# Kernel optimization log

Hardware: AMD Instinct MI355X
Metric: run time of the kernel (lower is better)

Reference implementation:

```python
import jax, jax.numpy as jnp
import numpy as np

H = 8      # hidden_size
IN = 14    # input_size
B = 4096   # batch
T = 512    # seq_len
BN_EPS = 1e-5


def setup_inputs() -> dict:
    key = jax.random.key(0)
    ks = jax.random.split(key, 16)
    s = lambda k, shape, scale=0.25: jax.random.normal(k, shape, jnp.float32) * scale
    return {
        "x": jax.random.normal(ks[0], (B, T, IN), jnp.float32),
        # layer 1 LSTM params (PyTorch gate order: i, f, g, o)
        "Wih1": s(ks[1], (4 * H, IN)), "Whh1": s(ks[2], (4 * H, H)),
        "bih1": s(ks[3], (4 * H,)), "bhh1": s(ks[4], (4 * H,)),
        # layer 2 LSTM params
        "Wih2": s(ks[5], (4 * H, H)), "Whh2": s(ks[6], (4 * H, H)),
        "bih2": s(ks[7], (4 * H,)), "bhh2": s(ks[8], (4 * H,)),
        # BatchNorm1d(H) params + running stats (eval mode)
        "bn_gamma": jnp.ones((H,), jnp.float32), "bn_beta": jnp.zeros((H,), jnp.float32),
        "bn_mean": s(ks[9], (H,), 0.01), "bn_var": jnp.ones((H,), jnp.float32),
        # MLP head
        "w1": s(ks[10], (4, H)), "b1": s(ks[11], (4,)),
        "w2": s(ks[12], (1, 4)), "b2": s(ks[13], (1,)),
    }


def _cell(gates, c):
    # gates: [B, 4H] pre-activation, PyTorch order i, f, g, o
    i, f, g, o = jnp.split(gates, 4, axis=-1)
    c_new = jax.nn.sigmoid(f) * c + jax.nn.sigmoid(i) * jnp.tanh(g)
    h_new = jax.nn.sigmoid(o) * jnp.tanh(c_new)
    return h_new, c_new


def _lstm_last(x, Wih1, Whh1, bih1, bhh1, Wih2, Whh2, bih2, bhh2):
    # x: [B, T, IN] -> returns last hidden state of layer 2: [B, H]
    xt = jnp.swapaxes(x, 0, 1)  # [T, B, IN]
    # precompute input projections for layer 1 in one big GEMM
    xp1 = jnp.einsum('tbf,gf->tbg', xt, Wih1) + (bih1 + bhh1)  # [T, B, 4H]
    b2sum = bih2 + bhh2
    Bn = x.shape[0]
    z = jnp.zeros((Bn, H), x.dtype)
    init = (z, z, z, z)  # h1, c1, h2, c2

    def step(carry, xp):
        h1, c1, h2, c2 = carry
        h1, c1 = _cell(xp + h1 @ Whh1.T, c1)
        h2, c2 = _cell(h1 @ Wih2.T + h2 @ Whh2.T + b2sum, c2)
        return (h1, c1, h2, c2), None

    (h1, c1, h2, c2), _ = jax.lax.scan(step, init, xp1)
    return h2


def reference(x, Wih1, Whh1, bih1, bhh1, Wih2, Whh2, bih2, bhh2,
              bn_gamma, bn_beta, bn_mean, bn_var, w1, b1, w2, b2):
    last = _lstm_last(x, Wih1, Whh1, bih1, bhh1, Wih2, Whh2, bih2, bhh2)  # [B, H]
    # BatchNorm1d in eval mode (running stats); dropout is identity in eval
    normed = bn_gamma * (last - bn_mean) / jnp.sqrt(bn_var + BN_EPS) + bn_beta
    h = jax.nn.relu(normed @ w1.T + b1)  # [B, 4]
    out = h @ w2.T + b2                  # [B, 1]
    return out.squeeze(-1)               # [B]
```

## Files before the change

### kernel.cpp

```cpp
#include <hip/hip_runtime.h>

#define T_SEQ 512
#define INPUT 14
#define HID 8
#define TC 16
#define NCHUNK (T_SEQ / TC)
#define BN_EPS 1e-5f

__device__ __forceinline__ float fast_exp2(float x) { return __builtin_amdgcn_exp2f(x); }
__device__ __forceinline__ float fast_rcp(float x)  { return __builtin_amdgcn_rcpf(x); }

template <int IMM>
__device__ __forceinline__ float swz(float v) {
    return __int_as_float(__builtin_amdgcn_ds_swizzle(__float_as_int(v), IMM));
}

#define DPP_XOR1 0xB1
#define DPP_XOR2 0x4E
#define DPP_XOR3 0x1B
#define DPP_XOR8 0x128
template <int CTRL>
__device__ __forceinline__ float dpp(float v) {
    return __int_as_float(__builtin_amdgcn_update_dpp(
        0, __float_as_int(v), CTRL, 0xF, 0xF, true));
}

__device__ __forceinline__ void butterfly8u(float h, float (&hx)[8]) {
    hx[0] = h;
    float x4  = swz<0x101F>(h);
    float x16 = swz<0x401F>(h);
    float x20 = swz<0x501F>(h);
    hx[1] = x4;
    hx[2] = dpp<DPP_XOR8>(h);
    hx[3] = dpp<DPP_XOR8>(x4);
    hx[4] = x16;
    hx[5] = x20;
    hx[6] = dpp<DPP_XOR8>(x16);
    hx[7] = dpp<DPP_XOR8>(x20);
}

__global__ __launch_bounds__(256, 2)
void lstm_forex_kernel(const float* __restrict__ x,
                       const float* __restrict__ Wih1, const float* __restrict__ Whh1,
                       const float* __restrict__ bih1, const float* __restrict__ bhh1,
                       const float* __restrict__ Wih2, const float* __restrict__ Whh2,
                       const float* __restrict__ bih2, const float* __restrict__ bhh2,
                       const float* __restrict__ bn_gamma, const float* __restrict__ bn_beta,
                       const float* __restrict__ bn_mean, const float* __restrict__ bn_var,
                       const float* __restrict__ w1p, const float* __restrict__ b1p,
                       const float* __restrict__ w2p, const float* __restrict__ b2p,
                       float* __restrict__ out)
{
    __shared__ float xbuf[4][2][TC][16];

    const int tid  = threadIdx.x;
    const int wave = tid >> 6;
    const int lane = tid & 63;
    const int grp  = lane >> 5;
    const int l5   = lane & 31;
    const int u    = (l5 >> 2) & 7;
    const int type = l5 & 3;
    const int row  = type * 8 + u;
    const bool b0  = (type & 1) != 0;
    const bool b1  = (type & 2) != 0;

    const int b = blockIdx.x * 8 + wave * 2 + grp;

    float wi1[INPUT], wh1p[8], wi2p[8], wh2p[8];
#pragma unroll
    for (int k = 0; k < INPUT; ++k) wi1[k] = Wih1[row * INPUT + k];
#pragma unroll
    for (int m = 0; m < 8; ++m) {
        int j = u ^ m;
        wh1p[m] = Whh1[row * HID + j];
        wi2p[m] = Wih2[row * HID + j];
        wh2p[m] = Whh2[row * HID + j];
    }
    const float bsum1 = bih1[row] + bhh1[row];
    const float bsum2 = bih2[row] + bhh2[row];

    const float actScale = (type == 2) ? -2.885390082f : -1.4426950408f;
    const float actMul   = (type == 2) ? 2.f : 1.f;
    const float actAdd   = (type == 2) ? -1.f : 0.f;

    const float* gptr[7];
    int loff[7];
#pragma unroll
    for (int it = 0; it < 7; ++it) {
        int d   = it * 64 + lane;
        int es  = d / 224;
        int idx = d - es * 224;
        int tr  = idx / 14;
        int k   = idx - tr * 14;
        int bb  = blockIdx.x * 8 + wave * 2 + es;
        gptr[it] = x + (size_t)bb * (T_SEQ * INPUT) + idx;
        loff[it] = es * (TC * 16) + tr * 16 + k;
    }

    float hx1[8], hx2[8];
    float c1 = 0.f, c2 = 0.f;
#pragma unroll
    for (int m = 0; m < 8; ++m) { hx1[m] = 0.f; hx2[m] = 0.f; }

    float st[7];
#pragma unroll
    for (int it = 0; it < 7; ++it) { st[it] = *gptr[it]; gptr[it] += TC * INPUT; }

    float (*xw)[TC][16] = xbuf[wave];

    for (int c = 0; c < NCHUNK; ++c) {
#pragma unroll
        for (int it = 0; it < 7; ++it) ((float*)xw)[loff[it]] = st[it];
        if (c + 1 < NCHUNK) {
#pragma unroll
            for (int it = 0; it < 7; ++it) { st[it] = *gptr[it]; gptr[it] += TC * INPUT; }
        }
        __builtin_amdgcn_wave_barrier();

#pragma unroll
        for (int t = 0; t < TC; ++t) {
            const float* xrow = &xw[grp][t][0];
            float4 xa = *(const float4*)(xrow + 0);
            float4 xb = *(const float4*)(xrow + 4);
            float4 xc = *(const float4*)(xrow + 8);
            float2 xd = *(const float2*)(xrow + 12);

            float a0 = bsum1, a1 = 0.f;
            a0 = fmaf(xa.x, wi1[0], a0);  a1 = fmaf(xa.y, wi1[1], a1);
            a0 = fmaf(xa.z, wi1[2], a0);  a1 = fmaf(xa.w, wi1[3], a1);
            a0 = fmaf(xb.x, wi1[4], a0);  a1 = fmaf(xb.y, wi1[5], a1);
            a0 = fmaf(xb.z, wi1[6], a0);  a1 = fmaf(xb.w, wi1[7], a1);
            a0 = fmaf(xc.x, wi1[8], a0);  a1 = fmaf(xc.y, wi1[9], a1);
            a0 = fmaf(xc.z, wi1[10], a0); a1 = fmaf(xc.w, wi1[11], a1);
            a0 = fmaf(xd.x, wi1[12], a0); a1 = fmaf(xd.y, wi1[13], a1);
            float q0 = bsum2, q1 = 0.f;
#pragma unroll
            for (int m = 0; m < 8; m += 2) {
                q0 = fmaf(hx2[m],     wh2p[m],     q0);
                q1 = fmaf(hx2[m + 1], wh2p[m + 1], q1);
            }
#pragma unroll
            for (int m = 0; m < 8; m += 2) {
                a0 = fmaf(hx1[m],     wh1p[m],     a0);
                a1 = fmaf(hx1[m + 1], wh1p[m + 1], a1);
            }
            float acc = a0 + a1;

            float v0 = fmaf(fast_rcp(1.f + fast_exp2(actScale * acc)), actMul, actAdd);
            float v1 = dpp<DPP_XOR1>(v0);
            float v2 = dpp<DPP_XOR2>(v0);
            float v3 = dpp<DPP_XOR3>(v0);
            float P = b0 ? v1 * v3 : v0 * v2;
            float A = b0 ? v0 : v1;
            float Bq = b0 ? v2 : v3;
            float F = b1 ? Bq : A;
            float O = b1 ? A : Bq;
            c1 = fmaf(F, c1, P);
            float th1 = fmaf(fast_rcp(1.f + fast_exp2(-2.885390082f * c1)), 2.f, -1.f);
            float h1u = O * th1;
            butterfly8u(h1u, hx1);

            float p0 = q0, p1 = q1;
#pragma unroll
            for (int m = 0; m < 8; m += 2) {
                p0 = fmaf(hx1[m],     wi2p[m],     p0);
                p1 = fmaf(hx1[m + 1], wi2p[m + 1], p1);
            }
            float acc2 = p0 + p1;

            float u0 = fmaf(fast_rcp(1.f + fast_exp2(actScale * acc2)), actMul, actAdd);
            float u1 = dpp<DPP_XOR1>(u0);
            float u2 = dpp<DPP_XOR2>(u0);
            float u3 = dpp<DPP_XOR3>(u0);
            float P2 = b0 ? u1 * u3 : u0 * u2;
            float A2 = b0 ? u0 : u1;
            float B2 = b0 ? u2 : u3;
            float F2 = b1 ? B2 : A2;
            float O2 = b1 ? A2 : B2;
            c2 = fmaf(F2, c2, P2);
            float th2 = fmaf(fast_rcp(1.f + fast_exp2(-2.885390082f * c2)), 2.f, -1.f);
            float h2u = O2 * th2;
            butterfly8u(h2u, hx2);
        }
    }

    if (l5 == 0) {
        float nd[HID];
#pragma unroll
        for (int j = 0; j < HID; ++j) {
            float inv = 1.f / sqrtf(bn_var[j] + BN_EPS);
            nd[j] = bn_gamma[j] * (hx2[j] - bn_mean[j]) * inv + bn_beta[j];
        }
        float acc = b2p[0];
#pragma unroll
        for (int m = 0; m < 4; ++m) {
            float s = b1p[m];
#pragma unroll
            for (int j = 0; j < HID; ++j) s = fmaf(nd[j], w1p[m * HID + j], s);
            s = fmaxf(s, 0.f);
            acc = fmaf(s, w2p[m], acc);
        }
        out[b] = acc;
    }
}

extern "C" void kernel_launch(void* const* d_in, const int* in_sizes, int n_in,
                              void* d_out, int out_size, void* d_ws, size_t ws_size,
                              hipStream_t stream) {
    const float* x        = (const float*)d_in[0];
    const float* Wih1     = (const float*)d_in[1];
    const float* Whh1     = (const float*)d_in[2];
    const float* bih1     = (const float*)d_in[3];
    const float* bhh1     = (const float*)d_in[4];
    const float* Wih2     = (const float*)d_in[5];
    const float* Whh2     = (const float*)d_in[6];
    const float* bih2     = (const float*)d_in[7];
    const float* bhh2     = (const float*)d_in[8];
    const float* bn_gamma = (const float*)d_in[9];
    const float* bn_beta  = (const float*)d_in[10];
    const float* bn_mean  = (const float*)d_in[11];
    const float* bn_var   = (const float*)d_in[12];
    const float* w1p      = (const float*)d_in[13];
    const float* b1p      = (const float*)d_in[14];
    const float* w2p      = (const float*)d_in[15];
    const float* b2p      = (const float*)d_in[16];
    float* out = (float*)d_out;

    const int B = in_sizes[0] / (T_SEQ * INPUT);
    dim3 grid(B / 8), block(256);
    hipLaunchKernelGGL(lstm_forex_kernel, grid, block, 0, stream,
                       x, Wih1, Whh1, bih1, bhh1, Wih2, Whh2, bih2, bhh2,
                       bn_gamma, bn_beta, bn_mean, bn_var, w1p, b1p, w2p, b2p, out);
}
```

Baseline: 339.8 us.

## Fold activation scales into weights, broadcast gates via DPP, pack input FMAs

Measured after the change: 328.7 us. 3.3% less time.

```diff
diff --git a/kernel.cpp b/kernel.cpp
--- a/kernel.cpp
+++ b/kernel.cpp
@@ -7,17 +7,31 @@
 #define NCHUNK (T_SEQ / TC)
 #define BN_EPS 1e-5f
 
+typedef float v2f __attribute__((ext_vector_type(2)));
+
 __device__ __forceinline__ float fast_exp2(float x) { return __builtin_amdgcn_exp2f(x); }
 __device__ __forceinline__ float fast_rcp(float x)  { return __builtin_amdgcn_rcpf(x); }
+
+__device__ __forceinline__ v2f pk_fma(v2f a, v2f b, v2f c) {
+    v2f d;
+    asm("v_pk_fma_f32 %0, %1, %2, %3" : "=v"(d) : "v"(a), "v"(b), "v"(c));
+    return d;
+}
+__device__ __forceinline__ v2f pk_mul(v2f a, v2f b) {
+    v2f d;
+    asm("v_pk_mul_f32 %0, %1, %2" : "=v"(d) : "v"(a), "v"(b));
+    return d;
+}
 
 template <int IMM>
 __device__ __forceinline__ float swz(float v) {
     return __int_as_float(__builtin_amdgcn_ds_swizzle(__float_as_int(v), IMM));
 }
 
-#define DPP_XOR1 0xB1
-#define DPP_XOR2 0x4E
-#define DPP_XOR3 0x1B
+#define DPP_BC0  0x00
+#define DPP_BC1  0x55
+#define DPP_BC2  0xAA
+#define DPP_BC3  0xFF
 #define DPP_XOR8 0x128
 template <int CTRL>
 __device__ __forceinline__ float dpp(float v) {
@@ -61,27 +75,30 @@
     const int u    = (l5 >> 2) & 7;
     const int type = l5 & 3;
     const int row  = type * 8 + u;
-    const bool b0  = (type & 1) != 0;
-    const bool b1  = (type & 2) != 0;
 
     const int b = blockIdx.x * 8 + wave * 2 + grp;
 
-    float wi1[INPUT], wh1p[8], wi2p[8], wh2p[8];
-#pragma unroll
-    for (int k = 0; k < INPUT; ++k) wi1[k] = Wih1[row * INPUT + k];
+    const float gateScale = (type == 2) ? -2.885390082f : -1.4426950408f;
+    const float actMul    = (type == 2) ? -5.770780164f : 1.f;
+    const float actAdd    = (type == 2) ?  2.885390082f : 0.f;
+
+    v2f   wi1p[7];
+    float wh1p[8], wi2p[8], wh2p[8];
+#pragma unroll
+    for (int k = 0; k < 7; ++k) {
+        wi1p[k] = (v2f){ Wih1[row * INPUT + 2 * k]     * gateScale,
+                         Wih1[row * INPUT + 2 * k + 1] * gateScale };
+    }
 #pragma unroll
     for (int m = 0; m < 8; ++m) {
         int j = u ^ m;
-        wh1p[m] = Whh1[row * HID + j];
-        wi2p[m] = Wih2[row * HID + j];
-        wh2p[m] = Whh2[row * HID + j];
-    }
-    const float bsum1 = bih1[row] + bhh1[row];
-    const float bsum2 = bih2[row] + bhh2[row];
-
-    const float actScale = (type == 2) ? -2.885390082f : -1.4426950408f;
-    const float actMul   = (type == 2) ? 2.f : 1.f;
-    const float actAdd   = (type == 2) ? -1.f : 0.f;
+        wh1p[m] = Whh1[row * HID + j] * gateScale;
+        wi2p[m] = Wih2[row * HID + j] * gateScale;
+        wh2p[m] = Whh2[row * HID + j] * gateScale;
+    }
+    const float bsum1s = (bih1[row] + bhh1[row]) * gateScale;
+    const float bsum2s = (bih2[row] + bhh2[row]) * gateScale;
+    const v2f   bias1  = { bsum1s, 0.f };
 
     const float* gptr[7];
     int loff[7];
@@ -125,61 +142,61 @@
             float4 xc = *(const float4*)(xrow + 8);
             float2 xd = *(const float2*)(xrow + 12);
 
-            float a0 = bsum1, a1 = 0.f;
-            a0 = fmaf(xa.x, wi1[0], a0);  a1 = fmaf(xa.y, wi1[1], a1);
-            a0 = fmaf(xa.z, wi1[2], a0);  a1 = fmaf(xa.w, wi1[3], a1);
-            a0 = fmaf(xb.x, wi1[4], a0);  a1 = fmaf(xb.y, wi1[5], a1);
-            a0 = fmaf(xb.z, wi1[6], a0);  a1 = fmaf(xb.w, wi1[7], a1);
-            a0 = fmaf(xc.x, wi1[8], a0);  a1 = fmaf(xc.y, wi1[9], a1);
-            a0 = fmaf(xc.z, wi1[10], a0); a1 = fmaf(xc.w, wi1[11], a1);
-            a0 = fmaf(xd.x, wi1[12], a0); a1 = fmaf(xd.y, wi1[13], a1);
-            float q0 = bsum2, q1 = 0.f;
-#pragma unroll
-            for (int m = 0; m < 8; m += 2) {
-                q0 = fmaf(hx2[m],     wh2p[m],     q0);
-                q1 = fmaf(hx2[m + 1], wh2p[m + 1], q1);
-            }
-#pragma unroll
-            for (int m = 0; m < 8; m += 2) {
-                a0 = fmaf(hx1[m],     wh1p[m],     a0);
-                a1 = fmaf(hx1[m + 1], wh1p[m + 1], a1);
-            }
-            float acc = a0 + a1;
-
-            float v0 = fmaf(fast_rcp(1.f + fast_exp2(actScale * acc)), actMul, actAdd);
-            float v1 = dpp<DPP_XOR1>(v0);
-            float v2 = dpp<DPP_XOR2>(v0);
-            float v3 = dpp<DPP_XOR3>(v0);
-            float P = b0 ? v1 * v3 : v0 * v2;
-            float A = b0 ? v0 : v1;
-            float Bq = b0 ? v2 : v3;
-            float F = b1 ? Bq : A;
-            float O = b1 ? A : Bq;
-            c1 = fmaf(F, c1, P);
-            float th1 = fmaf(fast_rcp(1.f + fast_exp2(-2.885390082f * c1)), 2.f, -1.f);
-            float h1u = O * th1;
+            v2f ax0 = pk_fma((v2f){xa.x, xa.y}, wi1p[0], bias1);
+            v2f ax1 = pk_mul((v2f){xa.z, xa.w}, wi1p[1]);
+            ax0 = pk_fma((v2f){xb.x, xb.y}, wi1p[2], ax0);
+            ax1 = pk_fma((v2f){xb.z, xb.w}, wi1p[3], ax1);
+            ax0 = pk_fma((v2f){xc.x, xc.y}, wi1p[4], ax0);
+            ax1 = pk_fma((v2f){xc.z, xc.w}, wi1p[5], ax1);
+            ax0 = pk_fma((v2f){xd.x, xd.y}, wi1p[6], ax0);
+
+            float q0 = fmaf(hx2[0], wh2p[0], bsum2s);
+            float q1 = hx2[1] * wh2p[1];
+            float q2 = hx2[2] * wh2p[2];
+            float q3 = hx2[3] * wh2p[3];
+            q0 = fmaf(hx2[4], wh2p[4], q0);
+            q1 = fmaf(hx2[5], wh2p[5], q1);
+            q2 = fmaf(hx2[6], wh2p[6], q2);
+            q3 = fmaf(hx2[7], wh2p[7], q3);
+
+            float a0 = fmaf(hx1[0], wh1p[0], ax0.x);
+            float a1 = fmaf(hx1[1], wh1p[1], ax0.y);
+            float a2 = fmaf(hx1[2], wh1p[2], ax1.x);
+            float a3 = fmaf(hx1[3], wh1p[3], ax1.y);
+            a0 = fmaf(hx1[4], wh1p[4], a0);
+            a1 = fmaf(hx1[5], wh1p[5], a1);
+            a2 = fmaf(hx1[6], wh1p[6], a2);
+            a3 = fmaf(hx1[7], wh1p[7], a3);
+            float acc = (a0 + a1) + (a2 + a3);
+
+            float v0 = fmaf(fast_rcp(1.f + fast_exp2(acc)), actMul, actAdd);
+            float vi = dpp<DPP_BC0>(v0);
+            float vf = dpp<DPP_BC1>(v0);
+            float vg = dpp<DPP_BC2>(v0);
+            float vo = dpp<DPP_BC3>(v0);
+            c1 = fmaf(vf, c1, vi * vg);
+            float th1 = fmaf(fast_rcp(1.f + fast_exp2(c1)), 2.f, -1.f);
+            float h1u = vo * th1;
             butterfly8u(h1u, hx1);
 
-            float p0 = q0, p1 = q1;
-#pragma unroll
-            for (int m = 0; m < 8; m += 2) {
-                p0 = fmaf(hx1[m],     wi2p[m],     p0);
-                p1 = fmaf(hx1[m + 1], wi2p[m + 1], p1);
-            }
-            float acc2 = p0 + p1;
-
-            float u0 = fmaf(fast_rcp(1.f + fast_exp2(actScale * acc2)), actMul, actAdd);
-            float u1 = dpp<DPP_XOR1>(u0);
-            float u2 = dpp<DPP_XOR2>(u0);
-            float u3 = dpp<DPP_XOR3>(u0);
-            float P2 = b0 ? u1 * u3 : u0 * u2;
-            float A2 = b0 ? u0 : u1;
-            float B2 = b0 ? u2 : u3;
-            float F2 = b1 ? B2 : A2;
-            float O2 = b1 ? A2 : B2;
-            c2 = fmaf(F2, c2, P2);
-            float th2 = fmaf(fast_rcp(1.f + fast_exp2(-2.885390082f * c2)), 2.f, -1.f);
-            float h2u = O2 * th2;
+            float p0 = fmaf(hx1[0], wi2p[0], q0);
+            float p1 = fmaf(hx1[1], wi2p[1], q1);
+            float p2 = fmaf(hx1[2], wi2p[2], q2);
+            float p3 = fmaf(hx1[3], wi2p[3], q3);
+            p0 = fmaf(hx1[4], wi2p[4], p0);
+            p1 = fmaf(hx1[5], wi2p[5], p1);
+            p2 = fmaf(hx1[6], wi2p[6], p2);
+            p3 = fmaf(hx1[7], wi2p[7], p3);
+            float acc2 = (p0 + p1) + (p2 + p3);
+
+            float u0 = fmaf(fast_rcp(1.f + fast_exp2(acc2)), actMul, actAdd);
+            float ui = dpp<DPP_BC0>(u0);
+            float uf = dpp<DPP_BC1>(u0);
+            float ug = dpp<DPP_BC2>(u0);
+            float uo = dpp<DPP_BC3>(u0);
+            c2 = fmaf(uf, c2, ui * ug);
+            float th2 = fmaf(fast_rcp(1.f + fast_exp2(c2)), 2.f, -1.f);
+            float h2u = uo * th2;
             butterfly8u(h2u, hx2);
         }
     }
```
